# Kernel tuning notes

Measured on AMD Instinct MI355X. Metric: run time of the kernel, lower is better.

The kernel has to match this reference:

```python
import jax, jax.numpy as jnp
import numpy as np

N0, N1, E, B = 100000, 100000, 800000, 1024
F0, F1 = 93, 43


def _gin(x, src, dst, w, b, n):
    # GINConv(eps=0): h_i = Lin(x_i + sum_{j->i} x_j)
    agg = jax.ops.segment_sum(x[src], dst, num_segments=n)
    return (x + agg) @ w + b


def _pool(x, batch, num_graphs):
    s = jax.ops.segment_sum(x, batch, num_segments=num_graphs)
    cnt = jax.ops.segment_sum(jnp.ones((x.shape[0],), x.dtype), batch, num_segments=num_graphs)
    mean = s / jnp.maximum(cnt, 1.0)[:, None]
    mx = jax.ops.segment_max(x, batch, num_segments=num_graphs)
    return jnp.concatenate([mean, mx], axis=1)


def _pairnorm(x, eps=1e-5):
    x = x - x.mean(axis=0, keepdims=True)
    return x / jnp.sqrt(eps + (x * x).sum(-1).mean())


def _bn(x, gamma, beta, eps=1e-5):
    mu = x.mean(axis=0, keepdims=True)
    var = x.var(axis=0, keepdims=True)
    return (x - mu) / jnp.sqrt(var + eps) * gamma + beta


def _branch(x, ei, batch, n, wc_a, bc_a, wc_b, bc_b, fg_w1, fg_b1, fg_w2, fg_b2, fg_g, fg_bt, ff_w1, ff_b1, ff_w2, ff_b2):
    src, dst = ei[0], ei[1]
    h = jax.nn.relu(_gin(x, src, dst, wc_a, bc_a, n))
    h = jax.nn.relu(_gin(h, src, dst, wc_b, bc_b, n))
    g = _pairnorm(_pool(h, batch, B))
    g = jax.nn.relu(g @ fg_w1 + fg_b1)
    g = _bn(g @ fg_w2 + fg_b2, fg_g, fg_bt)  # [B, 512]
    z = jax.nn.relu(g @ ff_w1 + ff_b1)
    z = jax.nn.sigmoid(z @ ff_w2 + ff_b2)  # [B, 2]
    return z[:, 0], z[:, 1], g


def setup_inputs() -> dict:
    key = jax.random.key(0)
    ks = iter(jax.random.split(key, 40))

    def lin(fan_in, fan_out):
        bnd = 1.0 / np.sqrt(fan_in)
        w = jax.random.uniform(next(ks), (fan_in, fan_out), jnp.float32, -bnd, bnd)
        b = jax.random.uniform(next(ks), (fan_out,), jnp.float32, -bnd, bnd)
        return w, b

    x0 = jax.random.normal(next(ks), (N0, F0), jnp.float32)
    x1 = jax.random.normal(next(ks), (N1, F1), jnp.float32)
    ei0 = jax.random.randint(next(ks), (2, E), 0, N0, jnp.int32)
    ei1 = jax.random.randint(next(ks), (2, E), 0, N1, jnp.int32)
    b0 = jnp.sort(jax.random.randint(next(ks), (N0,), 0, B, jnp.int32))
    b1 = jnp.sort(jax.random.randint(next(ks), (N1,), 0, B, jnp.int32))

    inp = {"x0": x0, "edge_index_0": ei0, "batch_0": b0, "x1": x1, "edge_index_1": ei1, "batch_1": b1}
    inp["w_c1"], inp["b_c1"] = lin(F0, F0)
    inp["w_c2"], inp["b_c2"] = lin(F0, F0 * 10)
    inp["w_c3"], inp["b_c3"] = lin(F1, F1)
    inp["w_c4"], inp["b_c4"] = lin(F1, F1 * 10)
    inp["fg0_w1"], inp["fg0_b1"] = lin(F0 * 10 * 2, 1024)
    inp["fg0_w2"], inp["fg0_b2"] = lin(1024, 512)
    inp["fg0_g"], inp["fg0_bt"] = jnp.ones((512,), jnp.float32), jnp.zeros((512,), jnp.float32)
    inp["fg1_w1"], inp["fg1_b1"] = lin(F1 * 10 * 2, 1024)
    inp["fg1_w2"], inp["fg1_b2"] = lin(1024, 512)
    inp["fg1_g"], inp["fg1_bt"] = jnp.ones((512,), jnp.float32), jnp.zeros((512,), jnp.float32)
    inp["ff0_w1"], inp["ff0_b1"] = lin(512, 256)
    inp["ff0_w2"], inp["ff0_b2"] = lin(256, 2)
    inp["ff1_w1"], inp["ff1_b1"] = lin(512, 256)
    inp["ff1_w2"], inp["ff1_b2"] = lin(256, 2)
    return inp


def reference(x0, edge_index_0, batch_0, x1, edge_index_1, batch_1,
              w_c1, b_c1, w_c2, b_c2, w_c3, b_c3, w_c4, b_c4,
              fg0_w1, fg0_b1, fg0_w2, fg0_b2, fg0_g, fg0_bt,
              fg1_w1, fg1_b1, fg1_w2, fg1_b2, fg1_g, fg1_bt,
              ff0_w1, ff0_b1, ff0_w2, ff0_b2,
              ff1_w1, ff1_b1, ff1_w2, ff1_b2):
    alpha, beta, xg0 = _branch(x0, edge_index_0, batch_0, N0, w_c1, b_c1, w_c2, b_c2,
                               fg0_w1, fg0_b1, fg0_w2, fg0_b2, fg0_g, fg0_bt,
                               ff0_w1, ff0_b1, ff0_w2, ff0_b2)
    alpha1, beta1, xg1 = _branch(x1, edge_index_1, batch_1, N1, w_c3, b_c3, w_c4, b_c4,
                                 fg1_w1, fg1_b1, fg1_w2, fg1_b2, fg1_g, fg1_bt,
                                 ff1_w1, ff1_b1, ff1_w2, ff1_b2)
    return (alpha, beta, xg0, xg1, alpha1, beta1)
```

## Files before the change

kernel.cpp:

```cpp
#include <hip/hip_runtime.h>
#include <hip/hip_bf16.h>
#include <math.h>

#define EDGES 800000
#define NNODES 100000
#define NGRAPH 1024
#define SCAN_B 256

typedef __attribute__((ext_vector_type(8))) short short8v;
typedef __attribute__((ext_vector_type(4))) float float4v;
typedef unsigned short ushort_t;

__device__ inline ushort_t f2bf(float f) {
  __hip_bfloat16 h = __float2bfloat16(f);
  return *reinterpret_cast<ushort_t*>(&h);
}
__device__ inline float bf2f(ushort_t u) {
  return __uint_as_float(((unsigned int)u) << 16);
}

__global__ __launch_bounds__(256) void deg_k(const int* __restrict__ dst,
                                             int* __restrict__ deg, int E) {
  int e = blockIdx.x * 256 + threadIdx.x;
  if (e < E) atomicAdd(&deg[dst[e]], 1);
}

__global__ __launch_bounds__(SCAN_B) void scan_block_k(const int* __restrict__ deg,
                                                       int* __restrict__ scanned,
                                                       int* __restrict__ bsum, int n) {
  __shared__ int tmp[SCAN_B];
  int b = blockIdx.x, t = threadIdx.x, i = b * SCAN_B + t;
  int v = (i < n) ? deg[i] : 0;
  tmp[t] = v;
  __syncthreads();
  for (int off = 1; off < SCAN_B; off <<= 1) {
    int x = (t >= off) ? tmp[t - off] : 0;
    __syncthreads();
    tmp[t] += x;
    __syncthreads();
  }
  if (i < n) scanned[i] = tmp[t] - v;
  if (t == SCAN_B - 1) bsum[b] = tmp[t];
}

__global__ __launch_bounds__(512) void scan_sums_k(int* __restrict__ bsum, int nb) {
  __shared__ int tmp[512];
  int t = threadIdx.x;
  int v = (t < nb) ? bsum[t] : 0;
  tmp[t] = v;
  __syncthreads();
  for (int off = 1; off < 512; off <<= 1) {
    int x = (t >= off) ? tmp[t - off] : 0;
    __syncthreads();
    tmp[t] += x;
    __syncthreads();
  }
  if (t < nb) bsum[t] = tmp[t] - v;
}

__global__ __launch_bounds__(256) void scan_add_k(const int* __restrict__ scanned,
                                                  const int* __restrict__ bsum,
                                                  int* __restrict__ rowstart, int n,
                                                  int total) {
  int i = blockIdx.x * 256 + threadIdx.x;
  if (i < n) rowstart[i] = scanned[i] + bsum[i / SCAN_B];
  if (i == 0) rowstart[n] = total;
}

#define NBMAX 512
__global__ __launch_bounds__(256) void bscatter_k(const int* __restrict__ src,
                                                  const int* __restrict__ dst,
                                                  const int* __restrict__ rowstart,
                                                  int* __restrict__ bcur,
                                                  int2* __restrict__ EB, int E,
                                                  int NB) {
  __shared__ int hist[NBMAX], run[NBMAX], lcur[NBMAX];
  int t = threadIdx.x;
  for (int b = t; b < NB; b += 256) {
    hist[b] = 0;
    lcur[b] = 0;
  }
  __syncthreads();
  int e0 = blockIdx.x * 4096;
  int e1 = min(E, e0 + 4096);
  for (int e = e0 + t; e < e1; e += 256) atomicAdd(&hist[dst[e] >> 8], 1);
  __syncthreads();
  for (int b = t; b < NB; b += 256)
    if (hist[b] > 0) run[b] = atomicAdd(&bcur[b], hist[b]);
  __syncthreads();
  for (int e = e0 + t; e < e1; e += 256) {
    int d = dst[e];
    int b = d >> 8;
    int l = atomicAdd(&lcur[b], 1);
    int pos = rowstart[b << 8] + run[b] + l;
    EB[pos] = make_int2(src[e], d);
  }
}

__global__ __launch_bounds__(256) void fill2_k(const int2* __restrict__ EB,
                                               const int* __restrict__ rowstart,
                                               int* __restrict__ cur,
                                               int* __restrict__ adj, int E) {
  int e = blockIdx.x * 256 + threadIdx.x;
  if (e >= E) return;
  int2 ed = EB[e];
  int p = rowstart[ed.y] + atomicAdd(&cur[ed.y], 1);
  adj[p] = ed.x;
}

__global__ __launch_bounds__(256) void gstart_k(const int* __restrict__ bat,
                                                int* __restrict__ gs, int N, int B) {
  int g = blockIdx.x * 256 + threadIdx.x;
  if (g > B) return;
  if (g == B) {
    gs[B] = N;
    return;
  }
  int lo = 0, hi = N;
  while (lo < hi) {
    int mid = (lo + hi) >> 1;
    if (bat[mid] < g) lo = mid + 1;
    else hi = mid;
  }
  gs[g] = lo;
}

template <int KP>
__global__ __launch_bounds__(256) void tobf16_k(const float* __restrict__ x,
                                                ushort_t* __restrict__ out, int M,
                                                int F) {
  long i = (long)blockIdx.x * 256 + threadIdx.x;
  if (i >= (long)M * KP) return;
  int r = (int)(i / KP), c = (int)(i % KP);
  float v = (c < F) ? x[(long)r * F + c] : 0.f;
  out[i] = f2bf(v);
}

template <int KP>
__global__ __launch_bounds__(256) void gather_k(const ushort_t* __restrict__ X,
                                                const int* __restrict__ rowstart,
                                                const int* __restrict__ adj,
                                                ushort_t* __restrict__ out, int M) {
  constexpr int CH = KP / 8;
  long tid = (long)blockIdx.x * 256 + threadIdx.x;
  if (tid >= (long)M * CH) return;
  int node = (int)(tid / CH), ch = (int)(tid % CH);
  int o = ch * 8;
  float acc[8];
  uint4 self = *(const uint4*)&X[(long)node * KP + o];
  {
    const unsigned int u[4] = {self.x, self.y, self.z, self.w};
#pragma unroll
    for (int i = 0; i < 4; ++i) {
      acc[2 * i] = __uint_as_float((u[i] & 0xFFFFu) << 16);
      acc[2 * i + 1] = __uint_as_float(u[i] & 0xFFFF0000u);
    }
  }
  int rs = rowstart[node], re = rowstart[node + 1];
  for (int e = rs; e < re; ++e) {
    int j = adj[e];
    uint4 v = *(const uint4*)&X[(long)j * KP + o];
    const unsigned int u[4] = {v.x, v.y, v.z, v.w};
#pragma unroll
    for (int i = 0; i < 4; ++i) {
      acc[2 * i] += __uint_as_float((u[i] & 0xFFFFu) << 16);
      acc[2 * i + 1] += __uint_as_float(u[i] & 0xFFFF0000u);
    }
  }
  uint4 r;
  unsigned int* p = &r.x;
#pragma unroll
  for (int i = 0; i < 4; ++i) {
    unsigned int lo = f2bf(acc[2 * i]);
    unsigned int hi = f2bf(acc[2 * i + 1]);
    p[i] = lo | (hi << 16);
  }
  *(uint4*)&out[(long)node * KP + o] = r;
}

__global__ __launch_bounds__(256) void wt_k(const float* __restrict__ W,
                                            ushort_t* __restrict__ WT, int K, int N,
                                            int KP, int Npad) {
  int i = blockIdx.x * 256 + threadIdx.x;
  if (i >= Npad * KP) return;
  int n = i / KP, k = i % KP;
  float v = (k < K && n < N) ? W[(long)k * N + n] : 0.f;
  WT[i] = f2bf(v);
}

template <int KP>
__global__ __launch_bounds__(256) void conv_gemm2_k(
    const ushort_t* __restrict__ A, const ushort_t* __restrict__ WT,
    const float* __restrict__ bias, ushort_t* __restrict__ Cout, int M, int Nc,
    int OW, int NT) {
  constexpr int NKS = KP / 32;
  int tid = threadIdx.x;
  int wid = tid >> 6, lane = tid & 63;
  int lr = lane & 15, q = lane >> 4;
  int lk = q * 8;
  int row0 = blockIdx.x * 64;
  int arow = row0 + wid * 16 + lr;

  short8v a[NKS];
  const ushort_t* ap = A + (long)arow * KP + lk;
#pragma unroll
  for (int ks = 0; ks < NKS; ++ks) a[ks] = *(const short8v*)(ap + ks * 32);

  for (int ct = 0; ct < NT; ++ct) {
    int col0 = ct * 64;
    float4v acc[4];
#pragma unroll
    for (int i = 0; i < 4; ++i) acc[i] = (float4v){0.f, 0.f, 0.f, 0.f};
#pragma unroll
    for (int ks = 0; ks < NKS; ++ks) {
#pragma unroll
      for (int nf = 0; nf < 4; ++nf) {
        short8v b =
            *(const short8v*)&WT[(long)(col0 + nf * 16 + lr) * KP + ks * 32 + lk];
        acc[nf] = __builtin_amdgcn_mfma_f32_16x16x32_bf16(a[ks], b, acc[nf], 0, 0, 0);
      }
    }
#pragma unroll
    for (int nf = 0; nf < 4; ++nf) {
      int gc = col0 + nf * 16 + lr;
      if (gc >= OW) continue;
      float bv = (gc < Nc) ? bias[gc] : 0.f;
#pragma unroll
      for (int i = 0; i < 4; ++i) {
        int gr = row0 + wid * 16 + q * 4 + i;
        if (gr < M) {
          float v = (gc < Nc) ? fmaxf(acc[nf][i] + bv, 0.f) : 0.f;
          Cout[(long)gr * OW + gc] = f2bf(v);
        }
      }
    }
  }
}

template <int KP, int NT>
__global__ __launch_bounds__(256) void conv_pool_k(
    const ushort_t* __restrict__ A, const ushort_t* __restrict__ WT,
    const float* __restrict__ bias, const int* __restrict__ gstart,
    float* __restrict__ pool, int Nc, int NCpool) {
  constexpr int NKS = KP / 32;
  constexpr int MAXR = 128;
  constexpr int CH = KP / 8;
  constexpr int LDW = KP + 8;
  constexpr int MAXT = (NT + 3) / 4;
  __shared__ ushort_t Asl[MAXR * LDW];

  int g = blockIdx.x;
  int rs = gstart[g], re = gstart[g + 1];
  int rows = re - rs;
  int tid = threadIdx.x;
  int wid = tid >> 6, lane = tid & 63;
  int lr = lane & 15, q = lane >> 4, lk = q * 8;

  float ssum[MAXT][4];
  float smax[MAXT][4];
#pragma unroll
  for (int t = 0; t < MAXT; ++t)
#pragma unroll
    for (int nf = 0; nf < 4; ++nf) {
      ssum[t][nf] = 0.f;
      smax[t][nf] = 0.f;
    }

  int nwin = (rows + MAXR - 1) / MAXR;
  for (int w = 0; w < nwin; ++w) {
    int base = rs + w * MAXR;
    int wr = min(MAXR, re - base);
    for (int i = tid; i < wr * CH; i += 256) {
      int r = i / CH, cc = i % CH;
      *(uint4*)&Asl[r * LDW + cc * 8] = *(const uint4*)&A[(long)(base + r) * KP + cc * 8];
    }
    __syncthreads();
    int nch = (wr + 15) / 16;
#pragma unroll
    for (int t = 0; t < MAXT; ++t) {
      int ct = wid + t * 4;
      if (ct < NT) {
        int col0 = ct * 64;
        short8v bfr[NKS][4];
        float bv[4];
#pragma unroll
        for (int nf = 0; nf < 4; ++nf) {
          int gc = col0 + nf * 16 + lr;
          bv[nf] = (gc < Nc) ? bias[gc] : 0.f;
#pragma unroll
          for (int ks = 0; ks < NKS; ++ks)
            bfr[ks][nf] =
                *(const short8v*)&WT[(long)(col0 + nf * 16 + lr) * KP + ks * 32 + lk];
        }
        float wsum[4][4], wmax[4][4];
#pragma unroll
        for (int nf = 0; nf < 4; ++nf)
#pragma unroll
          for (int i = 0; i < 4; ++i) {
            wsum[nf][i] = 0.f;
            wmax[nf][i] = 0.f;
          }
        for (int c = 0; c < nch; ++c) {
          float4v acc[4];
#pragma unroll
          for (int i = 0; i < 4; ++i) acc[i] = (float4v){0.f, 0.f, 0.f, 0.f};
#pragma unroll
          for (int ks = 0; ks < NKS; ++ks) {
            short8v a = *(const short8v*)&Asl[(c * 16 + lr) * LDW + ks * 32 + lk];
#pragma unroll
            for (int nf = 0; nf < 4; ++nf)
              acc[nf] = __builtin_amdgcn_mfma_f32_16x16x32_bf16(a, bfr[ks][nf],
                                                                acc[nf], 0, 0, 0);
          }
          int rbase = c * 16 + q * 4;
#pragma unroll
          for (int nf = 0; nf < 4; ++nf)
#pragma unroll
            for (int i = 0; i < 4; ++i) {
              float v = (rbase + i < wr) ? fmaxf(acc[nf][i] + bv[nf], 0.f) : 0.f;
              wsum[nf][i] += v;
              wmax[nf][i] = fmaxf(wmax[nf][i], v);
            }
        }
#pragma unroll
        for (int nf = 0; nf < 4; ++nf) {
          float s = (wsum[nf][0] + wsum[nf][1]) + (wsum[nf][2] + wsum[nf][3]);
          float m = fmaxf(fmaxf(wmax[nf][0], wmax[nf][1]),
                          fmaxf(wmax[nf][2], wmax[nf][3]));
          s += __shfl_xor(s, 16);
          s += __shfl_xor(s, 32);
          m = fmaxf(m, __shfl_xor(m, 16));
          m = fmaxf(m, __shfl_xor(m, 32));
          ssum[t][nf] += s;
          smax[t][nf] = fmaxf(smax[t][nf], m);
        }
      }
    }
    if (w + 1 < nwin) __syncthreads();
  }

  float inv = 1.f / fmaxf((float)rows, 1.f);
  if (q == 0) {
#pragma unroll
    for (int t = 0; t < MAXT; ++t) {
      int ct = wid + t * 4;
      if (ct < NT) {
#pragma unroll
        for (int nf = 0; nf < 4; ++nf) {
          int gc = ct * 64 + nf * 16 + lr;
          if (gc < Nc) {
            pool[(long)g * 2 * NCpool + gc] = ssum[t][nf] * inv;
            pool[(long)g * 2 * NCpool + NCpool + gc] = smax[t][nf];
          }
        }
      }
    }
  }
}

__global__ __launch_bounds__(256) void fc_mfma_k(const ushort_t* __restrict__ A,
                                                 const ushort_t* __restrict__ WT,
                                                 float* __restrict__ PART, int KP,
                                                 int Nc, int Kc) {
  int tid = threadIdx.x;
  int wid = tid >> 6, lane = tid & 63;
  int lr = lane & 15, q = lane >> 4, lk = q * 8;
  int row0 = blockIdx.y * 64, col0 = blockIdx.x * 64;
  int M = gridDim.y * 64;
  int kbeg = blockIdx.z * Kc;
  int arow = row0 + wid * 16 + lr;
  const ushort_t* ap = A + (long)arow * KP + kbeg + lk;
  const ushort_t* wp = WT + (long)col0 * KP + kbeg + lk;

  float4v acc[4];
#pragma unroll
  for (int i = 0; i < 4; ++i) acc[i] = (float4v){0.f, 0.f, 0.f, 0.f};

  for (int k0 = 0; k0 < Kc; k0 += 32) {
    short8v a = *(const short8v*)(ap + k0);
#pragma unroll
    for (int nf = 0; nf < 4; ++nf) {
      short8v b = *(const short8v*)(wp + (long)(nf * 16 + lr) * KP + k0);
      acc[nf] = __builtin_amdgcn_mfma_f32_16x16x32_bf16(a, b, acc[nf], 0, 0, 0);
    }
  }

  float* P = PART + (long)blockIdx.z * M * Nc;
#pragma unroll
  for (int nf = 0; nf < 4; ++nf) {
    int gc = col0 + nf * 16 + lr;
#pragma unroll
    for (int i = 0; i < 4; ++i) {
      int gr = row0 + wid * 16 + q * 4 + i;
      P[(long)gr * Nc + gc] = acc[nf][i];
    }
  }
}

__global__ __launch_bounds__(256) void sk_epi2_k(const float* __restrict__ PART,
                                                 const float* __restrict__ bias,
                                                 float* __restrict__ Cf,
                                                 ushort_t* __restrict__ Cb, int M,
                                                 int Nc, int SK, int relu) {
  long idx = (long)blockIdx.x * 256 + threadIdx.x;
  if (idx >= (long)M * Nc) return;
  int c = (int)(idx % Nc);
  float s = bias[c];
  for (int z = 0; z < SK; ++z) s += PART[(long)z * M * Nc + idx];
  if (relu) s = fmaxf(s, 0.f);
  if (Cf) Cf[idx] = s;
  if (Cb) Cb[idx] = f2bf(s);
}

__global__ __launch_bounds__(256) void colstat_part_k(const float* __restrict__ X,
                                                      float* __restrict__ PS,
                                                      float* __restrict__ ssqtot,
                                                      int Rows, int Cols, int CR) {
  __shared__ float sred[256];
  int c0 = blockIdx.x * 64;
  int chunk = blockIdx.y;
  int t = threadIdx.x;
  int c = c0 + (t & 63);
  int rg = t >> 6;
  int rbeg = chunk * CR, rend = min(Rows, rbeg + CR);
  float s = 0.f, s2 = 0.f;
  if (c < Cols) {
    for (int r = rbeg + rg; r < rend; r += 4) {
      float v = X[(long)r * Cols + c];
      s += v;
      s2 += v * v;
    }
  }
  sred[t] = s;
  __syncthreads();
  if (t < 64 && c0 + t < Cols)
    PS[(long)chunk * Cols + c0 + t] = sred[t] + sred[t + 64] + sred[t + 128] + sred[t + 192];
  for (int off = 32; off > 0; off >>= 1) s2 += __shfl_down(s2, off);
  if ((t & 63) == 0) atomicAdd(ssqtot, s2);
}

__global__ __launch_bounds__(256) void colstat_fin_k(const float* __restrict__ PS,
                                                     float* __restrict__ cm, int Rows,
                                                     int Cols, int nchunk) {
  int c = blockIdx.x * 256 + threadIdx.x;
  if (c >= Cols) return;
  float s = 0.f;
  for (int z = 0; z < nchunk; ++z) s += PS[(long)z * Cols + c];
  cm[c] = s / Rows;
}

__global__ __launch_bounds__(256) void pn_scale_k(const float* __restrict__ cm,
                                                  const float* __restrict__ ssqtot,
                                                  float* __restrict__ scale, int Rows,
                                                  int Cols) {
  __shared__ float red[256];
  int t = threadIdx.x;
  float s = 0.f;
  for (int i = t; i < Cols; i += 256) {
    float v = cm[i];
    s += v * v;
  }
  red[t] = s;
  __syncthreads();
  for (int off = 128; off > 0; off >>= 1) {
    if (t < off) red[t] += red[t + off];
    __syncthreads();
  }
  if (t == 0) {
    float ssq = ssqtot[0] - (float)Rows * red[0];
    scale[0] = 1.f / sqrtf(1e-5f + ssq / Rows);
  }
}

__global__ __launch_bounds__(256) void pn_apply2_k(const float* __restrict__ X,
                                                   const float* __restrict__ cm,
                                                   const float* __restrict__ scale,
                                                   ushort_t* __restrict__ outB,
                                                   int Rows, int Cols, int KP1) {
  long idx = (long)blockIdx.x * 256 + threadIdx.x;
  if (idx >= (long)Rows * KP1) return;
  int r = (int)(idx / KP1), c = (int)(idx % KP1);
  float v = 0.f;
  if (c < Cols) v = (X[(long)r * Cols + c] - cm[c]) * scale[0];
  outB[idx] = f2bf(v);
}

__global__ __launch_bounds__(256) void bn_part_k(const float* __restrict__ X,
                                                 float* __restrict__ PS,
                                                 float* __restrict__ PQ, int Rows,
                                                 int Cols, int CR) {
  __shared__ float s1[256], s2l[256];
  int c0 = blockIdx.x * 64;
  int chunk = blockIdx.y;
  int t = threadIdx.x;
  int c = c0 + (t & 63);
  int rg = t >> 6;
  int rbeg = chunk * CR, rend = min(Rows, rbeg + CR);
  float a = 0.f, b = 0.f;
  if (c < Cols) {
    for (int r = rbeg + rg; r < rend; r += 4) {
      float v = X[(long)r * Cols + c];
      a += v;
      b += v * v;
    }
  }
  s1[t] = a;
  s2l[t] = b;
  __syncthreads();
  if (t < 64 && c0 + t < Cols) {
    PS[(long)chunk * Cols + c0 + t] = s1[t] + s1[t + 64] + s1[t + 128] + s1[t + 192];
    PQ[(long)chunk * Cols + c0 + t] = s2l[t] + s2l[t + 64] + s2l[t + 128] + s2l[t + 192];
  }
}

__global__ __launch_bounds__(256) void bn_fin_k(const float* __restrict__ PS,
                                                const float* __restrict__ PQ,
                                                float* __restrict__ mu,
                                                float* __restrict__ var, int Rows,
                                                int Cols, int nchunk) {
  int c = blockIdx.x * 256 + threadIdx.x;
  if (c >= Cols) return;
  float s = 0.f, q = 0.f;
  for (int z = 0; z < nchunk; ++z) {
    s += PS[(long)z * Cols + c];
    q += PQ[(long)z * Cols + c];
  }
  float m = s / Rows;
  mu[c] = m;
  var[c] = q / Rows - m * m;
}

__global__ void bn_apply2_k(float* __restrict__ X, const float* __restrict__ mu,
                            const float* __restrict__ var, const float* __restrict__ g,
                            const float* __restrict__ b, ushort_t* __restrict__ XB16,
                            int Rows, int Cols) {
  long idx = (long)blockIdx.x * 256 + threadIdx.x;
  if (idx >= (long)Rows * Cols) return;
  int c = (int)(idx % Cols);
  float v = (X[idx] - mu[c]) / sqrtf(var[c] + 1e-5f) * g[c] + b[c];
  X[idx] = v;
  XB16[idx] = f2bf(v);
}

__global__ __launch_bounds__(64) void ff2_k(const ushort_t* __restrict__ Z,
                                            const float* __restrict__ W2,
                                            const float* __restrict__ b2,
                                            float* __restrict__ alpha,
                                            float* __restrict__ beta, int K) {
  int row = blockIdx.x;
  int t = threadIdx.x;
  float s0 = 0.f, s1 = 0.f;
  for (int k = t; k < K; k += 64) {
    float z = bf2f(Z[(long)row * K + k]);
    s0 += z * W2[2 * k];
    s1 += z * W2[2 * k + 1];
  }
  for (int off = 32; off > 0; off >>= 1) {
    s0 += __shfl_down(s0, off);
    s1 += __shfl_down(s1, off);
  }
  if (t == 0) {
    alpha[row] = 1.f / (1.f + expf(-(s0 + b2[0])));
    beta[row] = 1.f / (1.f + expf(-(s1 + b2[1])));
  }
}

template <int KP, int NTT>
static void run_branch(const float* x, const int* ei, const int* bat,
                       const float* wc1, const float* bc1, const float* wc2,
                       const float* bc2, const float* fgw1, const float* fgb1,
                       const float* fgw2, const float* fgb2, const float* fgg,
                       const float* fgbt, const float* ffw1, const float* ffb1,
                       const float* ffw2, const float* ffb2, int N, int F,
                       float* out_alpha, float* out_beta, float* out_xg,
                       ushort_t* XB, ushort_t* XA, ushort_t* H, ushort_t* WT,
                       int* deg, int* scanned, int* rowstart, int* cur, int* bsum,
                       int* bcur, int* adj, int* GS, float* POOL, float* CM,
                       float* MU, float* VAR, float* SSQ, float* PSUM, float* PSQ,
                       ushort_t* POOLB, ushort_t* WTF1, ushort_t* WTF2,
                       ushort_t* WTFF, ushort_t* G1B, ushort_t* XGB, ushort_t* Z1B,
                       float* PART, hipStream_t stream) {
  const int NC = F * 10;
  const int Bn = NGRAPH;
  const int* src = ei;
  const int* dst = ei + EDGES;
  const int MB = (N + 63) / 64;
  const int Mpad = MB * 64;
  const int nb = (N + SCAN_B - 1) / SCAN_B;
  const int NB = (N + 255) >> 8;

  int2* EB = (int2*)XB;
  hipMemsetAsync(deg, 0, (size_t)N * 4, stream);
  hipMemsetAsync(cur, 0, (size_t)N * 4, stream);
  hipMemsetAsync(bcur, 0, NBMAX * 4, stream);
  deg_k<<<(EDGES + 255) / 256, 256, 0, stream>>>(dst, deg, EDGES);
  scan_block_k<<<nb, SCAN_B, 0, stream>>>(deg, scanned, bsum, N);
  scan_sums_k<<<1, 512, 0, stream>>>(bsum, nb);
  scan_add_k<<<nb, 256, 0, stream>>>(scanned, bsum, rowstart, N, EDGES);
  bscatter_k<<<(EDGES + 4095) / 4096, 256, 0, stream>>>(src, dst, rowstart, bcur, EB, EDGES, NB);
  fill2_k<<<(EDGES + 255) / 256, 256, 0, stream>>>(EB, rowstart, cur, adj, EDGES);
  gstart_k<<<(NGRAPH + 256) / 256, 256, 0, stream>>>(bat, GS, N, NGRAPH);

  constexpr int CH = KP / 8;
  if (Mpad > N)
    hipMemsetAsync(XA + (size_t)N * KP, 0, (size_t)(Mpad - N) * KP * 2, stream);
  tobf16_k<KP><<<(int)(((long)N * KP + 255) / 256), 256, 0, stream>>>(x, XB, N, F);
  gather_k<KP><<<(int)(((long)N * CH + 255) / 256), 256, 0, stream>>>(XB, rowstart, adj, XA, N);
  wt_k<<<(((F + 63) / 64) * 64 * KP + 255) / 256, 256, 0, stream>>>(
      wc1, WT, F, F, KP, ((F + 63) / 64) * 64);
  conv_gemm2_k<KP><<<MB, 256, 0, stream>>>(XA, WT, bc1, H, N, F, KP, (KP + 63) / 64);
  gather_k<KP><<<(int)(((long)N * CH + 255) / 256), 256, 0, stream>>>(H, rowstart, adj, XA, N);
  int Npad2 = ((NC + 63) / 64) * 64;
  wt_k<<<(Npad2 * KP + 255) / 256, 256, 0, stream>>>(wc2, WT, F, NC, KP, Npad2);
  conv_pool_k<KP, NTT><<<NGRAPH, 256, 0, stream>>>(XA, WT, bc2, GS, POOL, NC, NC);

  int Cols = 2 * NC;
  const int NCH = 16, CR = NGRAPH / NCH;
  hipMemsetAsync(SSQ, 0, 8, stream);
  colstat_part_k<<<dim3((Cols + 63) / 64, NCH), 256, 0, stream>>>(POOL, PSUM, SSQ, Bn, Cols, CR);
  colstat_fin_k<<<(Cols + 255) / 256, 256, 0, stream>>>(PSUM, CM, Bn, Cols, NCH);
  pn_scale_k<<<1, 256, 0, stream>>>(CM, SSQ, SSQ + 1, Bn, Cols);

  int KP1 = ((Cols + 127) / 128) * 128;
  pn_apply2_k<<<(int)(((long)Bn * KP1 + 255) / 256), 256, 0, stream>>>(
      POOL, CM, SSQ + 1, POOLB, Bn, Cols, KP1);
  wt_k<<<(1024 * KP1 + 255) / 256, 256, 0, stream>>>(fgw1, WTF1, Cols, 1024, KP1, 1024);
  fc_mfma_k<<<dim3(16, 16, 4), 256, 0, stream>>>(POOLB, WTF1, PART, KP1, 1024, KP1 / 4);
  sk_epi2_k<<<(Bn * 1024 + 255) / 256, 256, 0, stream>>>(PART, fgb1, nullptr, G1B, Bn, 1024, 4, 1);
  wt_k<<<(512 * 1024 + 255) / 256, 256, 0, stream>>>(fgw2, WTF2, 1024, 512, 1024, 512);
  fc_mfma_k<<<dim3(8, 16, 4), 256, 0, stream>>>(G1B, WTF2, PART, 1024, 512, 256);
  sk_epi2_k<<<(Bn * 512 + 255) / 256, 256, 0, stream>>>(PART, fgb2, out_xg, nullptr, Bn, 512, 4, 0);
  bn_part_k<<<dim3(8, 8), 256, 0, stream>>>(out_xg, PSUM, PSQ, Bn, 512, 128);
  bn_fin_k<<<2, 256, 0, stream>>>(PSUM, PSQ, MU, VAR, Bn, 512, 8);
  bn_apply2_k<<<(Bn * 512 + 255) / 256, 256, 0, stream>>>(out_xg, MU, VAR, fgg, fgbt, XGB, Bn, 512);
  wt_k<<<(256 * 512 + 255) / 256, 256, 0, stream>>>(ffw1, WTFF, 512, 256, 512, 256);
  fc_mfma_k<<<dim3(4, 16, 8), 256, 0, stream>>>(XGB, WTFF, PART, 512, 256, 64);
  sk_epi2_k<<<(Bn * 256 + 255) / 256, 256, 0, stream>>>(PART, ffb1, nullptr, Z1B, Bn, 256, 8, 1);
  ff2_k<<<Bn, 64, 0, stream>>>(Z1B, ffw2, ffb2, out_alpha, out_beta, 256);
}

extern "C" void kernel_launch(void* const* d_in, const int* in_sizes, int n_in,
                              void* d_out, int out_size, void* d_ws, size_t ws_size,
                              hipStream_t stream) {
  if (n_in < 34) return;
  const float* x0 = (const float*)d_in[0];
  const int* ei0 = (const int*)d_in[1];
  const int* b0 = (const int*)d_in[2];
  const float* x1 = (const float*)d_in[3];
  const int* ei1 = (const int*)d_in[4];
  const int* b1 = (const int*)d_in[5];
  const float* w_c1 = (const float*)d_in[6];
  const float* b_c1 = (const float*)d_in[7];
  const float* w_c2 = (const float*)d_in[8];
  const float* b_c2 = (const float*)d_in[9];
  const float* w_c3 = (const float*)d_in[10];
  const float* b_c3 = (const float*)d_in[11];
  const float* w_c4 = (const float*)d_in[12];
  const float* b_c4 = (const float*)d_in[13];
  const float* fg0_w1 = (const float*)d_in[14];
  const float* fg0_b1 = (const float*)d_in[15];
  const float* fg0_w2 = (const float*)d_in[16];
  const float* fg0_b2 = (const float*)d_in[17];
  const float* fg0_g = (const float*)d_in[18];
  const float* fg0_bt = (const float*)d_in[19];
  const float* fg1_w1 = (const float*)d_in[20];
  const float* fg1_b1 = (const float*)d_in[21];
  const float* fg1_w2 = (const float*)d_in[22];
  const float* fg1_b2 = (const float*)d_in[23];
  const float* fg1_g = (const float*)d_in[24];
  const float* fg1_bt = (const float*)d_in[25];
  const float* ff0_w1 = (const float*)d_in[26];
  const float* ff0_b1 = (const float*)d_in[27];
  const float* ff0_w2 = (const float*)d_in[28];
  const float* ff0_b2 = (const float*)d_in[29];
  const float* ff1_w1 = (const float*)d_in[30];
  const float* ff1_b1 = (const float*)d_in[31];
  const float* ff1_w2 = (const float*)d_in[32];
  const float* ff1_b2 = (const float*)d_in[33];

  float* out = (float*)d_out;
  float* alpha = out;
  float* beta = out + 1024;
  float* xg0 = out + 2048;
  float* xg1 = out + 2048 + 1024 * 512;
  float* alpha1 = out + 2048 + 2 * 1024 * 512;
  float* beta1 = alpha1 + 1024;

  char* w = (char*)d_ws;
  auto alloc = [&](size_t bytes) -> void* {
    void* p = (void*)w;
    w += ((bytes + 255) / 256) * 256;
    return p;
  };
  const int Mpad = ((NNODES + 63) / 64) * 64;
  ushort_t* XB = (ushort_t*)alloc((size_t)Mpad * 96 * 2);
  ushort_t* XA = (ushort_t*)alloc((size_t)Mpad * 96 * 2);
  ushort_t* H = (ushort_t*)alloc((size_t)Mpad * 96 * 2);
  ushort_t* WT = (ushort_t*)alloc((size_t)960 * 96 * 2);
  int* deg = (int*)alloc((size_t)(NNODES + 1) * 4);
  int* scanned = (int*)alloc((size_t)(NNODES + 1) * 4);
  int* rowstart = (int*)alloc((size_t)(NNODES + 1) * 4);
  int* cur = (int*)alloc((size_t)NNODES * 4);
  int* bsum = (int*)alloc(512 * 4);
  int* bcur = (int*)alloc(NBMAX * 4);
  int* adj = (int*)alloc((size_t)EDGES * 4);
  int* GS = (int*)alloc((size_t)(NGRAPH + 1) * 4);
  float* POOL = (float*)alloc((size_t)NGRAPH * 1860 * 4);
  float* CM = (float*)alloc(1860 * 4);
  float* MU = (float*)alloc(512 * 4);
  float* VAR = (float*)alloc(512 * 4);
  float* SSQ = (float*)alloc(256);
  float* PSUM = (float*)alloc((size_t)16 * 1920 * 4);
  float* PSQ = (float*)alloc((size_t)8 * 512 * 4);
  ushort_t* POOLB = (ushort_t*)alloc((size_t)NGRAPH * 1920 * 2);
  ushort_t* WTF1 = (ushort_t*)alloc((size_t)1024 * 1920 * 2);
  ushort_t* WTF2 = (ushort_t*)alloc((size_t)512 * 1024 * 2);
  ushort_t* WTFF = (ushort_t*)alloc((size_t)256 * 512 * 2);
  ushort_t* G1B = (ushort_t*)alloc((size_t)NGRAPH * 1024 * 2);
  ushort_t* XGB = (ushort_t*)alloc((size_t)NGRAPH * 512 * 2);
  ushort_t* Z1B = (ushort_t*)alloc((size_t)NGRAPH * 256 * 2);
  if ((size_t)(w - (char*)d_ws) > ws_size) return;

  float* PART = (float*)XB;

  run_branch<96, 15>(x0, ei0, b0, w_c1, b_c1, w_c2, b_c2, fg0_w1, fg0_b1, fg0_w2,
                     fg0_b2, fg0_g, fg0_bt, ff0_w1, ff0_b1, ff0_w2, ff0_b2, NNODES,
                     93, alpha, beta, xg0, XB, XA, H, WT, deg, scanned, rowstart,
                     cur, bsum, bcur, adj, GS, POOL, CM, MU, VAR, SSQ, PSUM, PSQ,
                     POOLB, WTF1, WTF2, WTFF, G1B, XGB, Z1B, PART, stream);
  run_branch<64, 7>(x1, ei1, b1, w_c3, b_c3, w_c4, b_c4, fg1_w1, fg1_b1, fg1_w2,
                    fg1_b2, fg1_g, fg1_bt, ff1_w1, ff1_b1, ff1_w2, ff1_b2, NNODES,
                    43, alpha1, beta1, xg1, XB, XA, H, WT, deg, scanned, rowstart,
                    cur, bsum, bcur, adj, GS, POOL, CM, MU, VAR, SSQ, PSUM, PSQ,
                    POOLB, WTF1, WTF2, WTFF, G1B, XGB, Z1B, PART, stream);
}
```

Baseline: 721.2 us.

## Split conv+pool kernel across column tiles with single-wave blocks

Replaces the per-graph 256-thread conv+pool kernel, which staged rows in shared memory and looped over column tiles per wave, with a 2D grid (graph x 64-column tile) of one-wave blocks that read A rows directly from global memory. This removes the shared-memory staging and block syncs and exposes many more independent blocks to fill the GPU. In exchange, each graph's A rows are re-read once per column tile, relying on cache to absorb the repeated traffic. Rows past the graph end may be read from the next graph or padding, but they are masked out.

```diff
diff --git a/kernel.cpp b/kernel.cpp
--- a/kernel.cpp
+++ b/kernel.cpp
@@ -237,123 +237,73 @@
   }
 }
 
-template <int KP, int NT>
-__global__ __launch_bounds__(256) void conv_pool_k(
+template <int KP>
+__global__ __launch_bounds__(64) void conv_pool2_k(
     const ushort_t* __restrict__ A, const ushort_t* __restrict__ WT,
     const float* __restrict__ bias, const int* __restrict__ gstart,
     float* __restrict__ pool, int Nc, int NCpool) {
   constexpr int NKS = KP / 32;
-  constexpr int MAXR = 128;
-  constexpr int CH = KP / 8;
-  constexpr int LDW = KP + 8;
-  constexpr int MAXT = (NT + 3) / 4;
-  __shared__ ushort_t Asl[MAXR * LDW];
-
   int g = blockIdx.x;
+  int col0 = blockIdx.y * 64;
   int rs = gstart[g], re = gstart[g + 1];
   int rows = re - rs;
-  int tid = threadIdx.x;
-  int wid = tid >> 6, lane = tid & 63;
+  int lane = threadIdx.x;
   int lr = lane & 15, q = lane >> 4, lk = q * 8;
 
-  float ssum[MAXT][4];
-  float smax[MAXT][4];
-#pragma unroll
-  for (int t = 0; t < MAXT; ++t)
-#pragma unroll
-    for (int nf = 0; nf < 4; ++nf) {
-      ssum[t][nf] = 0.f;
-      smax[t][nf] = 0.f;
-    }
-
-  int nwin = (rows + MAXR - 1) / MAXR;
-  for (int w = 0; w < nwin; ++w) {
-    int base = rs + w * MAXR;
-    int wr = min(MAXR, re - base);
-    for (int i = tid; i < wr * CH; i += 256) {
-      int r = i / CH, cc = i % CH;
-      *(uint4*)&Asl[r * LDW + cc * 8] = *(const uint4*)&A[(long)(base + r) * KP + cc * 8];
-    }
-    __syncthreads();
-    int nch = (wr + 15) / 16;
-#pragma unroll
-    for (int t = 0; t < MAXT; ++t) {
-      int ct = wid + t * 4;
-      if (ct < NT) {
-        int col0 = ct * 64;
-        short8v bfr[NKS][4];
-        float bv[4];
-#pragma unroll
-        for (int nf = 0; nf < 4; ++nf) {
-          int gc = col0 + nf * 16 + lr;
-          bv[nf] = (gc < Nc) ? bias[gc] : 0.f;
-#pragma unroll
-          for (int ks = 0; ks < NKS; ++ks)
-            bfr[ks][nf] =
-                *(const short8v*)&WT[(long)(col0 + nf * 16 + lr) * KP + ks * 32 + lk];
-        }
-        float wsum[4][4], wmax[4][4];
-#pragma unroll
-        for (int nf = 0; nf < 4; ++nf)
-#pragma unroll
-          for (int i = 0; i < 4; ++i) {
-            wsum[nf][i] = 0.f;
-            wmax[nf][i] = 0.f;
-          }
-        for (int c = 0; c < nch; ++c) {
-          float4v acc[4];
-#pragma unroll
-          for (int i = 0; i < 4; ++i) acc[i] = (float4v){0.f, 0.f, 0.f, 0.f};
-#pragma unroll
-          for (int ks = 0; ks < NKS; ++ks) {
-            short8v a = *(const short8v*)&Asl[(c * 16 + lr) * LDW + ks * 32 + lk];
-#pragma unroll
-            for (int nf = 0; nf < 4; ++nf)
-              acc[nf] = __builtin_amdgcn_mfma_f32_16x16x32_bf16(a, bfr[ks][nf],
-                                                                acc[nf], 0, 0, 0);
-          }
-          int rbase = c * 16 + q * 4;
-#pragma unroll
-          for (int nf = 0; nf < 4; ++nf)
-#pragma unroll
-            for (int i = 0; i < 4; ++i) {
-              float v = (rbase + i < wr) ? fmaxf(acc[nf][i] + bv[nf], 0.f) : 0.f;
-              wsum[nf][i] += v;
-              wmax[nf][i] = fmaxf(wmax[nf][i], v);
-            }
-        }
-#pragma unroll
-        for (int nf = 0; nf < 4; ++nf) {
-          float s = (wsum[nf][0] + wsum[nf][1]) + (wsum[nf][2] + wsum[nf][3]);
-          float m = fmaxf(fmaxf(wmax[nf][0], wmax[nf][1]),
-                          fmaxf(wmax[nf][2], wmax[nf][3]));
-          s += __shfl_xor(s, 16);
-          s += __shfl_xor(s, 32);
-          m = fmaxf(m, __shfl_xor(m, 16));
-          m = fmaxf(m, __shfl_xor(m, 32));
-          ssum[t][nf] += s;
-          smax[t][nf] = fmaxf(smax[t][nf], m);
-        }
+  short8v bfr[NKS][4];
+  float bv[4];
+#pragma unroll
+  for (int nf = 0; nf < 4; ++nf) {
+    int gc = col0 + nf * 16 + lr;
+    bv[nf] = (gc < Nc) ? bias[gc] : 0.f;
+#pragma unroll
+    for (int ks = 0; ks < NKS; ++ks)
+      bfr[ks][nf] = *(const short8v*)&WT[(long)gc * KP + ks * 32 + lk];
+  }
+
+  float wsum[4][4] = {}, wmax[4][4] = {};
+  int nch = (rows + 15) / 16;
+  for (int c = 0; c < nch; ++c) {
+    const ushort_t* ap = A + (long)(rs + c * 16 + lr) * KP + lk;
+    short8v a[NKS];
+#pragma unroll
+    for (int ks = 0; ks < NKS; ++ks) a[ks] = *(const short8v*)(ap + ks * 32);
+    float4v acc[4];
+#pragma unroll
+    for (int i = 0; i < 4; ++i) acc[i] = (float4v){0.f, 0.f, 0.f, 0.f};
+#pragma unroll
+    for (int ks = 0; ks < NKS; ++ks)
+#pragma unroll
+      for (int nf = 0; nf < 4; ++nf)
+        acc[nf] = __builtin_amdgcn_mfma_f32_16x16x32_bf16(a[ks], bfr[ks][nf],
+                                                          acc[nf], 0, 0, 0);
+    int rbase = c * 16 + q * 4;
+#pragma unroll
+    for (int i = 0; i < 4; ++i) {
+      bool ok = rbase + i < rows;
+#pragma unroll
+      for (int nf = 0; nf < 4; ++nf) {
+        float v = ok ? fmaxf(acc[nf][i] + bv[nf], 0.f) : 0.f;
+        wsum[nf][i] += v;
+        wmax[nf][i] = fmaxf(wmax[nf][i], v);
       }
     }
-    if (w + 1 < nwin) __syncthreads();
   }
 
   float inv = 1.f / fmaxf((float)rows, 1.f);
-  if (q == 0) {
-#pragma unroll
-    for (int t = 0; t < MAXT; ++t) {
-      int ct = wid + t * 4;
-      if (ct < NT) {
-#pragma unroll
-        for (int nf = 0; nf < 4; ++nf) {
-          int gc = ct * 64 + nf * 16 + lr;
-          if (gc < Nc) {
-            pool[(long)g * 2 * NCpool + gc] = ssum[t][nf] * inv;
-            pool[(long)g * 2 * NCpool + NCpool + gc] = smax[t][nf];
-          }
-        }
-      }
+#pragma unroll
+  for (int nf = 0; nf < 4; ++nf) {
+    float s = (wsum[nf][0] + wsum[nf][1]) + (wsum[nf][2] + wsum[nf][3]);
+    float m = fmaxf(fmaxf(wmax[nf][0], wmax[nf][1]),
+                    fmaxf(wmax[nf][2], wmax[nf][3]));
+    s += __shfl_xor(s, 16);
+    s += __shfl_xor(s, 32);
+    m = fmaxf(m, __shfl_xor(m, 16));
+    m = fmaxf(m, __shfl_xor(m, 32));
+    int gc = col0 + nf * 16 + lr;
+    if (q == 0 && gc < Nc) {
+      pool[(long)g * 2 * NCpool + gc] = s * inv;
+      pool[(long)g * 2 * NCpool + NCpool + gc] = m;
     }
   }
 }
@@ -565,7 +515,7 @@
   }
 }
 
-template <int KP, int NTT>
+template <int KP>
 static void run_branch(const float* x, const int* ei, const int* bat,
                        const float* wc1, const float* bc1, const float* wc2,
                        const float* bc2, const float* fgw1, const float* fgb1,
@@ -612,7 +562,7 @@
   gather_k<KP><<<(int)(((long)N * CH + 255) / 256), 256, 0, stream>>>(H, rowstart, adj, XA, N);
   int Npad2 = ((NC + 63) / 64) * 64;
   wt_k<<<(Npad2 * KP + 255) / 256, 256, 0, stream>>>(wc2, WT, F, NC, KP, Npad2);
-  conv_pool_k<KP, NTT><<<NGRAPH, 256, 0, stream>>>(XA, WT, bc2, GS, POOL, NC, NC);
+  conv_pool2_k<KP><<<dim3(NGRAPH, Npad2 / 64), 64, 0, stream>>>(XA, WT, bc2, GS, POOL, NC, NC);
 
   int Cols = 2 * NC;
   const int NCH = 16, CR = NGRAPH / NCH;
@@ -723,14 +673,14 @@
 
   float* PART = (float*)XB;
 
-  run_branch<96, 15>(x0, ei0, b0, w_c1, b_c1, w_c2, b_c2, fg0_w1, fg0_b1, fg0_w2,
-                     fg0_b2, fg0_g, fg0_bt, ff0_w1, ff0_b1, ff0_w2, ff0_b2, NNODES,
-                     93, alpha, beta, xg0, XB, XA, H, WT, deg, scanned, rowstart,
-                     cur, bsum, bcur, adj, GS, POOL, CM, MU, VAR, SSQ, PSUM, PSQ,
-                     POOLB, WTF1, WTF2, WTFF, G1B, XGB, Z1B, PART, stream);
-  run_branch<64, 7>(x1, ei1, b1, w_c3, b_c3, w_c4, b_c4, fg1_w1, fg1_b1, fg1_w2,
-                    fg1_b2, fg1_g, fg1_bt, ff1_w1, ff1_b1, ff1_w2, ff1_b2, NNODES,
-                    43, alpha1, beta1, xg1, XB, XA, H, WT, deg, scanned, rowstart,
-                    cur, bsum, bcur, adj, GS, POOL, CM, MU, VAR, SSQ, PSUM, PSQ,
-                    POOLB, WTF1, WTF2, WTFF, G1B, XGB, Z1B, PART, stream);
-}
+  run_branch<96>(x0, ei0, b0, w_c1, b_c1, w_c2, b_c2, fg0_w1, fg0_b1, fg0_w2,
+                 fg0_b2, fg0_g, fg0_bt, ff0_w1, ff0_b1, ff0_w2, ff0_b2, NNODES,
+                 93, alpha, beta, xg0, XB, XA, H, WT, deg, scanned, rowstart,
+                 cur, bsum, bcur, adj, GS, POOL, CM, MU, VAR, SSQ, PSUM, PSQ,
+                 POOLB, WTF1, WTF2, WTFF, G1B, XGB, Z1B, PART, stream);
+  run_branch<64>(x1, ei1, b1, w_c3, b_c3, w_c4, b_c4, fg1_w1, fg1_b1, fg1_w2,
+                 fg1_b2, fg1_g, fg1_bt, ff1_w1, ff1_b1, ff1_w2, ff1_b2, NNODES,
+                 43, alpha1, beta1, xg1, XB, XA, H, WT, deg, scanned, rowstart,
+                 cur, bsum, bcur, adj, GS, POOL, CM, MU, VAR, SSQ, PSUM, PSQ,
+                 POOLB, WTF1, WTF2, WTFF, G1B, XGB, Z1B, PART, stream);
+}
```

Measured after the change: 720.1 us. Within noise of the previous version (-0.1%).
